# Optimization experiments

Hardware: AMD Instinct MI355X
Metric: run time of the kernel (lower is better)

Reference implementation:

```python
import jax, jax.numpy as jnp
import numpy as np

NMODELS, SZ_IN, SZ_OUT, B = 128, 256, 256, 4096

def setup_inputs() -> dict:
    key = jax.random.key(0)
    k1, k2, k3, k4 = jax.random.split(key, 4)
    inp = jax.random.normal(k1, (B, SZ_IN), dtype=jnp.float32)
    agent_ids = jax.random.randint(k2, (B,), 0, NMODELS, dtype=jnp.int32)
    # Embedding tables (init ~ N(0,1) like nn.Embedding default)
    weight_lut = jax.random.normal(k3, (NMODELS, SZ_IN * SZ_OUT), dtype=jnp.float32)
    bias_lut = jax.random.normal(k4, (NMODELS, SZ_OUT), dtype=jnp.float32)
    return {"inp": inp, "agent_ids": agent_ids, "weight_lut": weight_lut, "bias_lut": bias_lut}

def reference(inp, agent_ids, weight_lut, bias_lut):
    # per-id weight gather -> [B, sz_in, sz_out]
    W = weight_lut[agent_ids].reshape(-1, SZ_IN, SZ_OUT)
    b = bias_lut[agent_ids]  # [B, sz_out]
    out = jnp.einsum('bi,bio->bo', inp, W) + b
    return out
```

## Files before the change

### kernel.cpp

```cpp
#include <hip/hip_runtime.h>

#define NMODELS 128
#define SZ_IN 256
#define SZ_OUT 256
#define CHUNK 16
#define MAXCHUNKS 384
#define LDSK 264

typedef __attribute__((ext_vector_type(4))) float f32x4;
typedef __attribute__((ext_vector_type(8))) short bf16x8;
typedef __attribute__((ext_vector_type(4))) short s16x4;

__device__ __forceinline__ short f2bf(float f) {
  union { float f; unsigned u; } v;
  v.f = f;
  const unsigned r = v.u + 0x7FFFu + ((v.u >> 16) & 1u);
  return (short)(r >> 16);
}

__global__ __launch_bounds__(256) void prep_v8(const int* __restrict__ ids, int B,
                                               int* __restrict__ sorted,
                                               int* __restrict__ cm,
                                               int* __restrict__ cs0,
                                               int* __restrict__ ccnt,
                                               int* __restrict__ ncp) {
  __shared__ int cnt[NMODELS];
  __shared__ int scan[NMODELS];
  __shared__ int pos[NMODELS];
  const int t = threadIdx.x;
  if (t < NMODELS) cnt[t] = 0;
  __syncthreads();
  const int4* idv = (const int4*)ids;
  const int n4 = B >> 2;
  for (int e = t; e < n4; e += 256) {
    const int4 r = idv[e];
    atomicAdd(&cnt[r.x], 1);
    atomicAdd(&cnt[r.y], 1);
    atomicAdd(&cnt[r.z], 1);
    atomicAdd(&cnt[r.w], 1);
  }
  __syncthreads();
  if (t < NMODELS) {
    const int c = cnt[t];
    scan[t] = c + ((((c + CHUNK - 1) / CHUNK) & 0xFFFF) << 16);
  }
  __syncthreads();
  for (int d = 1; d < NMODELS; d <<= 1) {
    int add = 0;
    if (t < NMODELS && t >= d) add = scan[t - d];
    __syncthreads();
    if (t < NMODELS) scan[t] += add;
    __syncthreads();
  }
  if (t == 0) *ncp = scan[NMODELS - 1] >> 16;
  if (t < NMODELS) {
    const int n = cnt[t];
    const int nch = (n + CHUNK - 1) / CHUNK;
    const int off_m = (scan[t] & 0xFFFF) - n;
    const int coff_m = (scan[t] >> 16) - nch;
    pos[t] = off_m;
    for (int c = 0; c < nch; ++c) {
      cm[coff_m + c] = t;
      cs0[coff_m + c] = off_m + c * CHUNK;
      const int rem = n - c * CHUNK;
      ccnt[coff_m + c] = rem < CHUNK ? rem : CHUNK;
    }
  }
  __syncthreads();
  for (int e = t; e < n4; e += 256) {
    const int4 r = idv[e];
    const int b = e * 4;
    sorted[atomicAdd(&pos[r.x], 1)] = b;
    sorted[atomicAdd(&pos[r.y], 1)] = b + 1;
    sorted[atomicAdd(&pos[r.z], 1)] = b + 2;
    sorted[atomicAdd(&pos[r.w], 1)] = b + 3;
  }
}

__global__ __launch_bounds__(256, 4) void linmulti_v8(
    const float* __restrict__ inp, const float* __restrict__ wlut,
    const float* __restrict__ blut, const int* __restrict__ sorted,
    const int* __restrict__ cm, const int* __restrict__ cs0,
    const int* __restrict__ ccnt, const int* __restrict__ ncp,
    float* __restrict__ out) {
  const int cj = blockIdx.x >> 1;
  if (cj >= *ncp) return;
  const int ch = blockIdx.x & 1;
  const int m = cm[cj];
  const int s0 = cs0[cj];
  const int scnt = ccnt[cj];
  const int tid = threadIdx.x;

  __shared__ short As[CHUNK * LDSK];
  __shared__ int sidx[CHUNK];

  if (tid < CHUNK) {
    const int p = (tid < scnt) ? tid : (scnt - 1);
    sidx[tid] = sorted[s0 + p];
  }
  __syncthreads();
#pragma unroll
  for (int v = 0; v < 4; ++v) {
    const int e4 = v * 256 + tid;
    const int s = e4 >> 6, f4 = e4 & 63;
    const f32x4 a = ((const f32x4*)(inp + (size_t)sidx[s] * SZ_IN))[f4];
    s16x4 h;
#pragma unroll
    for (int j = 0; j < 4; ++j) h[j] = f2bf(a[j]);
    *(s16x4*)(As + s * LDSK + f4 * 4) = h;
  }
  __syncthreads();

  const int lane = tid & 63;
  const int wv = tid >> 6;
  const int q = lane >> 4;
  const int n16 = lane & 15;
  const int colbase = ch * 128 + wv * 32;
  const float* __restrict__ Wm = wlut + (size_t)m * (SZ_IN * SZ_OUT);

  f32x4 acc[2];
  acc[0] = (f32x4){0.f, 0.f, 0.f, 0.f};
  acc[1] = (f32x4){0.f, 0.f, 0.f, 0.f};

#pragma unroll 2
  for (int k0 = 0; k0 < SZ_IN; k0 += 32) {
    const int ka = k0 + q * 8;
    const bf16x8 afr = *(const bf16x8*)(As + (n16)*LDSK + ka);
    float bw[2][8];
#pragma unroll
    for (int t = 0; t < 2; ++t) {
      const float* __restrict__ Bp = Wm + (size_t)ka * SZ_OUT + colbase + t * 16 + n16;
#pragma unroll
      for (int j = 0; j < 8; ++j) bw[t][j] = Bp[(size_t)j * SZ_OUT];
    }
#pragma unroll
    for (int t = 0; t < 2; ++t) {
      bf16x8 bfr;
#pragma unroll
      for (int j = 0; j < 8; ++j) bfr[j] = f2bf(bw[t][j]);
      acc[t] = __builtin_amdgcn_mfma_f32_16x16x32_bf16(afr, bfr, acc[t], 0, 0, 0);
    }
  }

#pragma unroll
  for (int t = 0; t < 2; ++t) {
    const int col = colbase + t * 16 + n16;
    const float bias_c = blut[m * SZ_OUT + col];
#pragma unroll
    for (int r = 0; r < 4; ++r) {
      const int srow = q * 4 + r;
      if (srow < scnt) {
        out[(size_t)sidx[srow] * SZ_OUT + col] = acc[t][r] + bias_c;
      }
    }
  }
}

extern "C" void kernel_launch(void* const* d_in, const int* in_sizes, int n_in,
                              void* d_out, int out_size, void* d_ws, size_t ws_size,
                              hipStream_t stream) {
  const float* inp = (const float*)d_in[0];
  const int* ids = (const int*)d_in[1];
  const float* wlut = (const float*)d_in[2];
  const float* blut = (const float*)d_in[3];
  float* out = (float*)d_out;
  const int B = in_sizes[1];

  int* w = (int*)d_ws;
  int* sorted = w;
  int* cm = w + 4096;
  int* cs0 = cm + MAXCHUNKS;
  int* ccnt = cs0 + MAXCHUNKS;
  int* ncp = ccnt + MAXCHUNKS;

  prep_v8<<<1, 256, 0, stream>>>(ids, B, sorted, cm, cs0, ccnt, ncp);
  linmulti_v8<<<2 * MAXCHUNKS, 256, 0, stream>>>(inp, wlut, blut, sorted, cm,
                                                 cs0, ccnt, ncp, out);
}
```

Before: 96.04 us.

## Pre-convert weight table to bf16 MFMA-fragment layout in prep kernel

The prep kernel gains 4096 extra blocks that convert the whole fp32 weight table to bf16. It stores the result in a tiled layout matching the 16x16x32 MFMA B-fragment order, while one remaining block still does the id sort. The main kernel then loads each B fragment as one contiguous 16-byte vector instead of eight strided fp32 loads plus per-element conversion, and launch bounds drop to 3 waves per SIMD. This trades redundant strided reads and conversions in the GEMM for an extra full pass over the 32MB table plus a 16MB bf16 write each call.

```diff
diff --git a/kernel.cpp b/kernel.cpp
--- a/kernel.cpp
+++ b/kernel.cpp
@@ -6,6 +6,7 @@
 #define CHUNK 16
 #define MAXCHUNKS 384
 #define LDSK 264
+#define NCVTBLK 4096
 
 typedef __attribute__((ext_vector_type(4))) float f32x4;
 typedef __attribute__((ext_vector_type(8))) short bf16x8;
@@ -18,16 +19,28 @@
   return (short)(r >> 16);
 }
 
-__global__ __launch_bounds__(256) void prep_v8(const int* __restrict__ ids, int B,
-                                               int* __restrict__ sorted,
-                                               int* __restrict__ cm,
-                                               int* __restrict__ cs0,
-                                               int* __restrict__ ccnt,
-                                               int* __restrict__ ncp) {
+__global__ __launch_bounds__(256) void prep_wcvt_v9(
+    const int* __restrict__ ids, int B, const float* __restrict__ wlut,
+    short* __restrict__ wsW, int* __restrict__ sorted, int* __restrict__ cm,
+    int* __restrict__ cs0, int* __restrict__ ccnt, int* __restrict__ ncp) {
+  const int t = threadIdx.x;
+  if (blockIdx.x < NCVTBLK) {
+    const int T = blockIdx.x * 4 + (t >> 6);
+    const int l = t & 63;
+    const int q = l >> 4, n16 = l & 15;
+    const int m = T >> 7, kb = (T >> 4) & 7, nt = T & 15;
+    const float* __restrict__ src =
+        wlut + ((size_t)m << 16) + (size_t)(kb * 32 + q * 8) * SZ_OUT + nt * 16 + n16;
+    bf16x8 h;
+#pragma unroll
+    for (int j = 0; j < 8; ++j) h[j] = f2bf(src[(size_t)j * SZ_OUT]);
+    *(bf16x8*)(wsW + (size_t)T * 512 + l * 8) = h;
+    return;
+  }
+
   __shared__ int cnt[NMODELS];
   __shared__ int scan[NMODELS];
   __shared__ int pos[NMODELS];
-  const int t = threadIdx.x;
   if (t < NMODELS) cnt[t] = 0;
   __syncthreads();
   const int4* idv = (const int4*)ids;
@@ -77,8 +90,8 @@
   }
 }
 
-__global__ __launch_bounds__(256, 4) void linmulti_v8(
-    const float* __restrict__ inp, const float* __restrict__ wlut,
+__global__ __launch_bounds__(256, 3) void linmulti_v9(
+    const float* __restrict__ inp, const short* __restrict__ wsW,
     const float* __restrict__ blut, const int* __restrict__ sorted,
     const int* __restrict__ cm, const int* __restrict__ cs0,
     const int* __restrict__ ccnt, const int* __restrict__ ncp,
@@ -115,36 +128,25 @@
   const int wv = tid >> 6;
   const int q = lane >> 4;
   const int n16 = lane & 15;
-  const int colbase = ch * 128 + wv * 32;
-  const float* __restrict__ Wm = wlut + (size_t)m * (SZ_IN * SZ_OUT);
+  const int nt0 = ch * 8 + wv * 2;
+  const short* __restrict__ Wb = wsW + ((size_t)m << 16) + lane * 8 + nt0 * 512;
 
   f32x4 acc[2];
   acc[0] = (f32x4){0.f, 0.f, 0.f, 0.f};
   acc[1] = (f32x4){0.f, 0.f, 0.f, 0.f};
 
-#pragma unroll 2
-  for (int k0 = 0; k0 < SZ_IN; k0 += 32) {
-    const int ka = k0 + q * 8;
-    const bf16x8 afr = *(const bf16x8*)(As + (n16)*LDSK + ka);
-    float bw[2][8];
-#pragma unroll
-    for (int t = 0; t < 2; ++t) {
-      const float* __restrict__ Bp = Wm + (size_t)ka * SZ_OUT + colbase + t * 16 + n16;
-#pragma unroll
-      for (int j = 0; j < 8; ++j) bw[t][j] = Bp[(size_t)j * SZ_OUT];
-    }
-#pragma unroll
-    for (int t = 0; t < 2; ++t) {
-      bf16x8 bfr;
-#pragma unroll
-      for (int j = 0; j < 8; ++j) bfr[j] = f2bf(bw[t][j]);
-      acc[t] = __builtin_amdgcn_mfma_f32_16x16x32_bf16(afr, bfr, acc[t], 0, 0, 0);
-    }
+#pragma unroll 4
+  for (int kb = 0; kb < 8; ++kb) {
+    const bf16x8 afr = *(const bf16x8*)(As + n16 * LDSK + kb * 32 + q * 8);
+    const bf16x8 b0 = *(const bf16x8*)(Wb + (size_t)kb * 8192);
+    const bf16x8 b1 = *(const bf16x8*)(Wb + (size_t)kb * 8192 + 512);
+    acc[0] = __builtin_amdgcn_mfma_f32_16x16x32_bf16(afr, b0, acc[0], 0, 0, 0);
+    acc[1] = __builtin_amdgcn_mfma_f32_16x16x32_bf16(afr, b1, acc[1], 0, 0, 0);
   }
 
 #pragma unroll
   for (int t = 0; t < 2; ++t) {
-    const int col = colbase + t * 16 + n16;
+    const int col = (nt0 + t) * 16 + n16;
     const float bias_c = blut[m * SZ_OUT + col];
 #pragma unroll
     for (int r = 0; r < 4; ++r) {
@@ -172,8 +174,10 @@
   int* cs0 = cm + MAXCHUNKS;
   int* ccnt = cs0 + MAXCHUNKS;
   int* ncp = ccnt + MAXCHUNKS;
+  short* wsW = (short*)(w + 8192);
 
-  prep_v8<<<1, 256, 0, stream>>>(ids, B, sorted, cm, cs0, ccnt, ncp);
-  linmulti_v8<<<2 * MAXCHUNKS, 256, 0, stream>>>(inp, wlut, blut, sorted, cm,
+  prep_wcvt_v9<<<NCVTBLK + 1, 256, 0, stream>>>(ids, B, wlut, wsW, sorted, cm,
+                                                cs0, ccnt, ncp);
+  linmulti_v9<<<2 * MAXCHUNKS, 256, 0, stream>>>(inp, wsW, blut, sorted, cm,
                                                  cs0, ccnt, ncp, out);
 }
```

Result: no change. 96.28 us (+0.3%).
